# Kernel tuning notes

Measured on AMD Instinct MI355X. Metric: run time of the kernel, lower is better.

Reference implementation:

```python
import jax, jax.numpy as jnp
import numpy as np


def setup_inputs() -> dict:
    key = jax.random.key(0)
    kx, kw = jax.random.split(key)
    B, C, H, W, K = 16, 256, 128, 128, 7
    x = jax.random.normal(kx, (B, C, H, W), dtype=jnp.float32)
    # module initializes w with uniform(-0.1, 0.1)
    w = jax.random.uniform(kw, (C, K, K), dtype=jnp.float32, minval=-0.1, maxval=0.1)
    return {"x": x, "w": w}


def reference(x, w):
    # PolarConv2D forward intent: unfold(2,K,S).unfold(3,K,S) then per-channel
    # contraction of each (K,K) patch with w[c] -> depthwise convolution.
    # out[b,c,i,j] = sum_{k1,k2} x[b,c,i*S+k1, j*S+k2] * w[c,k1,k2]
    # Implemented as a grouped conv (feature_group_count=C) so the K*K-times
    # redundant unfolded tensor is never materialized.
    C = w.shape[0]
    kern = w[:, None, :, :]  # OIHW with I=1 (depthwise)
    out = jax.lax.conv_general_dilated(
        x, kern,
        window_strides=(1, 1),
        padding="VALID",
        dimension_numbers=("NCHW", "OIHW", "NCHW"),
        feature_group_count=C,
    )
    return out  # (B, C, H-K+1, W-K+1)
```

## Files before the change

### kernel.cpp

```cpp
#include <hip/hip_runtime.h>


#define BATCH 16
#define CHAN  256
#define H_IN  128
#define W_IN  128
#define KS    7
#define H_OUT 122
#define W_OUT 122

typedef float v2f __attribute__((ext_vector_type(2)));

__device__ __forceinline__ float sgpr_bcast(float v) {
    return __int_as_float(__builtin_amdgcn_readfirstlane(__float_as_int(v)));
}

__global__ __launch_bounds__(256)
void dwconv7x7_kernel(const float* __restrict__ x,
                      const float* __restrict__ w,
                      float* __restrict__ out) {
    const int lane = threadIdx.x & 63;
    const int unit = blockIdx.x * 4 + (threadIdx.x >> 6);
    const int img  = unit >> 1;
    const int rh   = unit & 1;
    const int ch   = img & (CHAN - 1);

    int c = 2 * lane;
    if (lane >= 32) c -= 6;
    const int r0 = rh ? (H_IN - 70) : 0;

    const float* __restrict__ wp = w + ch * (KS * KS);
    float wr[KS * KS];
    #pragma unroll
    for (int i = 0; i < KS * KS; ++i) wr[i] = sgpr_bcast(wp[i]);

    const float* __restrict__ xq =
        x + (size_t)img * (H_IN * W_IN) + (size_t)r0 * W_IN + c;
    float* __restrict__ oq =
        out + (size_t)img * (H_OUT * W_OUT) + (size_t)r0 * W_OUT + c;

    float acc[KS][2] = {};
    float f[8];

    #define LOADW() do {                                                   \
        const v2f a0 = *reinterpret_cast<const v2f*>(xq);                  \
        const v2f a1 = *reinterpret_cast<const v2f*>(xq + 2);              \
        const v2f a2 = *reinterpret_cast<const v2f*>(xq + 4);              \
        const v2f a3 = *reinterpret_cast<const v2f*>(xq + 6);              \
        f[0] = a0.x; f[1] = a0.y; f[2] = a1.x; f[3] = a1.y;                \
        f[4] = a2.x; f[5] = a2.y; f[6] = a3.x; f[7] = a3.y; } while (0)

    #define ACCUM(SLOT, KY) do {                                           \
        _Pragma("unroll")                                                  \
        for (int kx = 0; kx < 7; ++kx) {                                   \
            const float wv = wr[(KY) * 7 + kx];                            \
            acc[(SLOT)][0] = fmaf(f[kx],     wv, acc[(SLOT)][0]);          \
            acc[(SLOT)][1] = fmaf(f[kx + 1], wv, acc[(SLOT)][1]);          \
        } } while (0)

    #pragma unroll
    for (int s = 0; s < 6; ++s) {
        LOADW();
        #pragma unroll
        for (int ky = 0; ky <= s; ++ky)
            ACCUM((s - ky) % KS, ky);
        xq += W_IN;
    }

    for (int sb = 0; sb < 9; ++sb) {
        #pragma unroll
        for (int u = 0; u < 7; ++u) {
            LOADW();
            #pragma unroll
            for (int ky = 0; ky < KS; ++ky)
                ACCUM((6 + u - ky + 7) % KS, ky);
            v2f v; v.x = acc[u][0]; v.y = acc[u][1];
            __builtin_nontemporal_store(v, reinterpret_cast<v2f*>(oq));
            acc[u][0] = 0.f; acc[u][1] = 0.f;
            xq += W_IN; oq += W_OUT;
        }
    }

    {
        LOADW();
        #pragma unroll
        for (int ky = 0; ky < KS; ++ky)
            ACCUM((6 - ky + 7) % KS, ky);
        v2f v; v.x = acc[0][0]; v.y = acc[0][1];
        __builtin_nontemporal_store(v, reinterpret_cast<v2f*>(oq));
    }

    #undef LOADW
    #undef ACCUM
}

extern "C" void kernel_launch(void* const* d_in, const int* in_sizes, int n_in,
                              void* d_out, int out_size, void* d_ws, size_t ws_size,
                              hipStream_t stream) {
    const float* x = (const float*)d_in[0];
    const float* w = (const float*)d_in[1];
    float* out = (float*)d_out;

    dim3 grid(8192 / 4, 1, 1);
    dim3 block(256, 1, 1);
    dwconv7x7_kernel<<<grid, block, 0, stream>>>(x, w, out);
}
```

Before: 99.32 us.

## Split each image across four waves of one block instead of two half-image waves

Each block now handles a single channel image, with its four waves each computing a 32-row output strip starting at row 30*q. Before, each wave covered half an image. This doubles the number of waves and shortens each wave's serial row loop, which should improve latency hiding and tail balance. The cost is more halo rows read from input (about 152 rows per image versus 140), though those reads come from the same block and are likely L2-friendly. It also leaves some overlapping output rows written twice.

```diff
diff --git a/kernel.cpp b/kernel.cpp
--- a/kernel.cpp
+++ b/kernel.cpp
@@ -20,14 +20,13 @@
                       const float* __restrict__ w,
                       float* __restrict__ out) {
     const int lane = threadIdx.x & 63;
-    const int unit = blockIdx.x * 4 + (threadIdx.x >> 6);
-    const int img  = unit >> 1;
-    const int rh   = unit & 1;
+    const int img  = blockIdx.x;
+    const int q    = threadIdx.x >> 6;
     const int ch   = img & (CHAN - 1);
 
     int c = 2 * lane;
     if (lane >= 32) c -= 6;
-    const int r0 = rh ? (H_IN - 70) : 0;
+    const int r0 = 30 * q;
 
     const float* __restrict__ wp = w + ch * (KS * KS);
     float wr[KS * KS];
@@ -58,6 +57,16 @@
             acc[(SLOT)][1] = fmaf(f[kx + 1], wv, acc[(SLOT)][1]);          \
         } } while (0)
 
+    #define MAINSTEP(U) do {                                               \
+        LOADW();                                                           \
+        _Pragma("unroll")                                                  \
+        for (int ky = 0; ky < KS; ++ky)                                    \
+            ACCUM((6 + (U) - ky + 7) % KS, ky);                            \
+        v2f v; v.x = acc[(U)][0]; v.y = acc[(U)][1];                       \
+        __builtin_nontemporal_store(v, reinterpret_cast<v2f*>(oq));        \
+        acc[(U)][0] = 0.f; acc[(U)][1] = 0.f;                              \
+        xq += W_IN; oq += W_OUT; } while (0)
+
     #pragma unroll
     for (int s = 0; s < 6; ++s) {
         LOADW();
@@ -67,31 +76,21 @@
         xq += W_IN;
     }
 
-    for (int sb = 0; sb < 9; ++sb) {
+    for (int sb = 0; sb < 4; ++sb) {
         #pragma unroll
         for (int u = 0; u < 7; ++u) {
-            LOADW();
-            #pragma unroll
-            for (int ky = 0; ky < KS; ++ky)
-                ACCUM((6 + u - ky + 7) % KS, ky);
-            v2f v; v.x = acc[u][0]; v.y = acc[u][1];
-            __builtin_nontemporal_store(v, reinterpret_cast<v2f*>(oq));
-            acc[u][0] = 0.f; acc[u][1] = 0.f;
-            xq += W_IN; oq += W_OUT;
+            MAINSTEP(u);
         }
     }
 
-    {
-        LOADW();
-        #pragma unroll
-        for (int ky = 0; ky < KS; ++ky)
-            ACCUM((6 - ky + 7) % KS, ky);
-        v2f v; v.x = acc[0][0]; v.y = acc[0][1];
-        __builtin_nontemporal_store(v, reinterpret_cast<v2f*>(oq));
+    #pragma unroll
+    for (int t = 0; t < 4; ++t) {
+        MAINSTEP(t);
     }
 
     #undef LOADW
     #undef ACCUM
+    #undef MAINSTEP
 }
 
 extern "C" void kernel_launch(void* const* d_in, const int* in_sizes, int n_in,
@@ -101,7 +100,7 @@
     const float* w = (const float*)d_in[1];
     float* out = (float*)d_out;
 
-    dim3 grid(8192 / 4, 1, 1);
+    dim3 grid(BATCH * CHAN, 1, 1);
     dim3 block(256, 1, 1);
     dwconv7x7_kernel<<<grid, block, 0, stream>>>(x, w, out);
 }
```

After: 95.44 us. -3.9%, faster.
